# Optimization experiments

Measured on AMD Instinct MI355X. Metric: run time of the kernel, lower is better.

## Reference

```python
import jax, jax.numpy as jnp
import numpy as np

TEMPERATURE = 1.0
IGNORE_INDEX = -100


def setup_inputs() -> dict:
    key = jax.random.key(0)
    k1, k2, k3 = jax.random.split(key, 3)
    N, V = 8192, 32000
    Q, D = 8192, 512
    return {
        "input": jax.random.normal(k1, (N, V), dtype=jnp.float32),
        "label": jax.random.randint(k2, (N,), 0, V, dtype=jnp.int64),
        "query": jax.random.normal(k3, (Q, D), dtype=jnp.float32),
    }


def _cross_entropy(logits, label):
    # nn.CrossEntropyLoss(ignore_index=IGNORE_INDEX): mean NLL over non-ignored.
    logp = jax.nn.log_softmax(logits, axis=-1)
    safe_label = jnp.clip(label, 0, logits.shape[-1] - 1)
    nll = -jnp.take_along_axis(logp, safe_label[:, None], axis=-1)[:, 0]
    valid = (label != IGNORE_INDEX)
    num_valid = jnp.maximum(jnp.sum(valid), 1)
    return jnp.sum(jnp.where(valid, nll, 0.0)) / num_valid.astype(logits.dtype)


def _query_similarity_penalty(query, temperature):
    sq_norm = jnp.sum(query * query, axis=-1)  # [Q]
    sq = sq_norm[:, None] + sq_norm[None, :] - 2.0 * (query @ query.T)
    sq = jnp.maximum(sq, 0.0)
    dist = jnp.sqrt(jnp.where(sq > 0.0, sq, 1.0))
    dist = jnp.where(sq > 0.0, dist, 0.0)  # exact 0 on diagonal
    sim = jnp.exp(-dist / temperature)
    return jnp.sqrt(jnp.sum(sim * sim))  # Frobenius norm


def reference(input, label, query):
    ce = _cross_entropy(input, label)
    penalty = _query_similarity_penalty(query, TEMPERATURE)
    return ce + penalty
```

## Files before the change

kernel.cpp:

```cpp
#include <hip/hip_runtime.h>
#include <hip/hip_bf16.h>
#include <cstdint>

typedef unsigned short u16;
typedef __attribute__((ext_vector_type(8))) short short8;
typedef __attribute__((ext_vector_type(4))) float floatx4;

#define IGNORE_INDEX (-100)

__global__ __launch_bounds__(64) void init_acc(float* acc) {
    if (threadIdx.x < 3) acc[threadIdx.x] = 0.f;
}

__global__ __launch_bounds__(256) void prep_kernel(const float* __restrict__ q,
                                                   u16* __restrict__ qb,
                                                   float* __restrict__ nrm) {
    const int gwave = (blockIdx.x * 256 + threadIdx.x) >> 6;
    const int lane  = threadIdx.x & 63;
    const float4* src = (const float4*)(q + (size_t)gwave * 512);
    float4 a = src[lane * 2];
    float4 b = src[lane * 2 + 1];
    float v[8] = {a.x, a.y, a.z, a.w, b.x, b.y, b.z, b.w};
    float ss = 0.f;
    union { u16 u[8]; uint4 p; } pk;
#pragma unroll
    for (int t = 0; t < 8; ++t) {
        ss += v[t] * v[t];
        __hip_bfloat16 h = __float2bfloat16(v[t]);
        pk.u[t] = *(u16*)&h;
    }
    ((uint4*)qb)[(size_t)gwave * 64 + lane] = pk.p;
#pragma unroll
    for (int off = 32; off; off >>= 1) ss += __shfl_down(ss, off);
    if (lane == 0) nrm[gwave] = ss;
}

#define GLD16(g, l) __builtin_amdgcn_global_load_lds(                          \
    (const __attribute__((address_space(1))) void*)(g),                        \
    (__attribute__((address_space(3))) void*)(l), 16, 0, 0)

__global__ __launch_bounds__(256, 2) void fused_kernel(const u16* __restrict__ qb,
                                                       const float* __restrict__ nrm,
                                                       const float* __restrict__ x,
                                                       const int* __restrict__ lab,
                                                       float* __restrict__ accs,
                                                       int V, int tiles_per_side) {
    __shared__ __align__(16) u16 At[128 * 64];
    __shared__ __align__(16) u16 Bt[128 * 64];
    __shared__ float red[4];
    const int bid  = blockIdx.x;
    const int tid  = threadIdx.x;
    const int lane = tid & 63;
    const int w    = tid >> 6;

    if (bid % 3 == 0) {
        const int t  = bid / 3;
        const int i0 = (t / tiles_per_side) * 128;
        const int j0 = (t % tiles_per_side) * 128;
        const int wr = w >> 1, wc = w & 1;
        const int m15 = lane & 15, quad = lane >> 4;

        floatx4 acc[4][4];
#pragma unroll
        for (int a = 0; a < 4; ++a)
#pragma unroll
            for (int b = 0; b < 4; ++b) acc[a][b] = (floatx4)0.f;

        for (int kt = 0; kt < 8; ++kt) {
            const int k0 = kt * 64;
#pragma unroll
            for (int it = 0; it < 4; ++it) {
                int c   = it * 256 + tid;
                int row = c >> 3;
                int kc  = (c & 7) ^ (row & 7);
                const u16* ga = qb + (size_t)(i0 + row) * 512 + k0 + kc * 8;
                const u16* gb = qb + (size_t)(j0 + row) * 512 + k0 + kc * 8;
                GLD16(ga, &At[c * 8]);
                GLD16(gb, &Bt[c * 8]);
            }
            __syncthreads();
#pragma unroll
            for (int ks = 0; ks < 2; ++ks) {
                const int kcq = ks * 4 + quad;
                short8 af[4], bfr[4];
#pragma unroll
                for (int f = 0; f < 4; ++f) {
                    int ra = wr * 64 + f * 16 + m15;
                    af[f]  = *(const short8*)&At[(ra * 8 + (kcq ^ (ra & 7))) * 8];
                    int rb = wc * 64 + f * 16 + m15;
                    bfr[f] = *(const short8*)&Bt[(rb * 8 + (kcq ^ (rb & 7))) * 8];
                }
#pragma unroll
                for (int fi = 0; fi < 4; ++fi)
#pragma unroll
                    for (int fj = 0; fj < 4; ++fj)
                        acc[fi][fj] = __builtin_amdgcn_mfma_f32_16x16x32_bf16(
                            af[fi], bfr[fj], acc[fi][fj], 0, 0, 0);
            }
            __syncthreads();
        }

        float ni[4][4], nj[4];
#pragma unroll
        for (int fi = 0; fi < 4; ++fi)
#pragma unroll
            for (int r = 0; r < 4; ++r)
                ni[fi][r] = nrm[i0 + wr * 64 + fi * 16 + quad * 4 + r];
#pragma unroll
        for (int fj = 0; fj < 4; ++fj) nj[fj] = nrm[j0 + wc * 64 + fj * 16 + m15];

        float lsum = 0.f;
#pragma unroll
        for (int fi = 0; fi < 4; ++fi) {
#pragma unroll
            for (int fj = 0; fj < 4; ++fj) {
#pragma unroll
                for (int r = 0; r < 4; ++r) {
                    int i = i0 + wr * 64 + fi * 16 + quad * 4 + r;
                    int j = j0 + wc * 64 + fj * 16 + m15;
                    float sq = ni[fi][r] + nj[fj] - 2.f * acc[fi][fj][r];
                    float s;
                    if (i == j) s = 1.f;
                    else if (sq > 0.f) s = __expf(-sqrtf(sq));
                    else s = 1.f;
                    lsum += s * s;
                }
            }
        }
#pragma unroll
        for (int off = 32; off; off >>= 1) lsum += __shfl_down(lsum, off);
        if (lane == 0) red[w] = lsum;
        __syncthreads();
        if (tid == 0) atomicAdd(&accs[0], red[0] + red[1] + red[2] + red[3]);
    } else {
        const int row = bid - bid / 3 - 1;
        const float* xr = x + (size_t)row * V;
        float s = 0.f;
        const int nvec = V >> 2;
        const float4* xv = (const float4*)xr;
        for (int idx = tid; idx < nvec; idx += 256) {
            float4 v = xv[idx];
            s += __expf(v.x) + __expf(v.y) + __expf(v.z) + __expf(v.w);
        }
        for (int idx = (nvec << 2) + tid; idx < V; idx += 256)
            s += __expf(xr[idx]);
#pragma unroll
        for (int off = 32; off; off >>= 1) s += __shfl_down(s, off);
        if (lane == 0) red[w] = s;
        __syncthreads();
        if (tid == 0) {
            float S = red[0] + red[1] + red[2] + red[3];
            int l = lab[row];
            if (l != IGNORE_INDEX) {
                float xl = xr[l];
                atomicAdd(&accs[1], __logf(S) - xl);
                atomicAdd(&accs[2], 1.f);
            }
        }
    }
}

__global__ void finalize_kernel(const float* __restrict__ accs, float* __restrict__ out) {
    out[0] = accs[1] / fmaxf(accs[2], 1.f) + sqrtf(accs[0]);
}

extern "C" void kernel_launch(void* const* d_in, const int* in_sizes, int n_in,
                              void* d_out, int out_size, void* d_ws, size_t ws_size,
                              hipStream_t stream) {
    const float* input = (const float*)d_in[0];
    const int*   label = (const int*)d_in[1];
    const float* query = (const float*)d_in[2];
    float* out = (float*)d_out;

    const int N = in_sizes[1];
    const int V = in_sizes[0] / N;
    const int D = 512;
    const int Q = in_sizes[2] / D;
    const int T = Q / 128;

    float* accs = (float*)d_ws;
    float* nrm  = (float*)((char*)d_ws + 4096);
    u16*   qb   = (u16*)  ((char*)d_ws + 4096 + 64 * 1024);

    hipLaunchKernelGGL(init_acc, dim3(1), dim3(64), 0, stream, accs);
    hipLaunchKernelGGL(prep_kernel, dim3(Q / 4), dim3(256), 0, stream, query, qb, nrm);
    hipLaunchKernelGGL(fused_kernel, dim3(T * T + N), dim3(256), 0, stream,
                       qb, nrm, input, label, accs, V, T);
    hipLaunchKernelGGL(finalize_kernel, dim3(1), dim3(1), 0, stream, accs, out);
}
```

Baseline: 1.417 ms.

## Exploit symmetry of distance matrix and unroll CE row reduction with nontemporal loads

The pairwise similarity sum now visits only upper-triangular tiles, doubling off-diagonal tile contributions, which roughly halves the GEMM and exp work. The interleave ratio between GEMM tiles and CE rows changes from 1:2 to 1:4 to keep the mix balanced, and excess CE blocks exit early. The CE row loop is unrolled 8-way with nontemporal vector loads and split accumulators, and the label gather is issued before the streaming loop. The linear search for the triangular tile index adds a small per-block cost.

```diff
diff --git a/kernel.cpp b/kernel.cpp
--- a/kernel.cpp
+++ b/kernel.cpp
@@ -44,7 +44,7 @@
                                                        const float* __restrict__ x,
                                                        const int* __restrict__ lab,
                                                        float* __restrict__ accs,
-                                                       int V, int tiles_per_side) {
+                                                       int V, int N, int tiles_per_side) {
     __shared__ __align__(16) u16 At[128 * 64];
     __shared__ __align__(16) u16 Bt[128 * 64];
     __shared__ float red[4];
@@ -53,10 +53,13 @@
     const int lane = tid & 63;
     const int w    = tid >> 6;
 
-    if (bid % 3 == 0) {
-        const int t  = bid / 3;
-        const int i0 = (t / tiles_per_side) * 128;
-        const int j0 = (t % tiles_per_side) * 128;
+    if (bid % 5 == 0) {
+        int t = bid / 5;
+        int ti = 0, rem = t;
+        while (rem >= tiles_per_side - ti) { rem -= tiles_per_side - ti; ++ti; }
+        const int tj = ti + rem;
+        const int i0 = ti * 128;
+        const int j0 = tj * 128;
         const int wr = w >> 1, wc = w & 1;
         const int m15 = lane & 15, quad = lane >> 4;
 
@@ -131,28 +134,53 @@
         for (int off = 32; off; off >>= 1) lsum += __shfl_down(lsum, off);
         if (lane == 0) red[w] = lsum;
         __syncthreads();
-        if (tid == 0) atomicAdd(&accs[0], red[0] + red[1] + red[2] + red[3]);
+        if (tid == 0) {
+            const float wgt = (ti == tj) ? 1.f : 2.f;
+            atomicAdd(&accs[0], wgt * (red[0] + red[1] + red[2] + red[3]));
+        }
     } else {
-        const int row = bid - bid / 3 - 1;
+        const int row = bid - bid / 5 - 1;
+        if (row >= N) return;
         const float* xr = x + (size_t)row * V;
-        float s = 0.f;
+
+        int l = 0; float xl = 0.f;
+        if (tid == 0) {
+            l = lab[row];
+            if (l != IGNORE_INDEX) xl = xr[l];
+        }
+
         const int nvec = V >> 2;
-        const float4* xv = (const float4*)xr;
-        for (int idx = tid; idx < nvec; idx += 256) {
-            float4 v = xv[idx];
-            s += __expf(v.x) + __expf(v.y) + __expf(v.z) + __expf(v.w);
-        }
-        for (int idx = (nvec << 2) + tid; idx < V; idx += 256)
-            s += __expf(xr[idx]);
+        const floatx4* __restrict__ xv = (const floatx4*)xr;
+        float s0 = 0.f, s1 = 0.f, s2 = 0.f, s3 = 0.f;
+        int idx = tid;
+        const int lim = nvec - 256 * 7;
+        for (; idx < lim; idx += 256 * 8) {
+            floatx4 v[8];
+#pragma unroll
+            for (int u = 0; u < 8; ++u)
+                v[u] = __builtin_nontemporal_load(xv + idx + 256 * u);
+#pragma unroll
+            for (int u = 0; u < 8; ++u) {
+                s0 += __expf(v[u].x);
+                s1 += __expf(v[u].y);
+                s2 += __expf(v[u].z);
+                s3 += __expf(v[u].w);
+            }
+        }
+        for (; idx < nvec; idx += 256) {
+            floatx4 v = __builtin_nontemporal_load(xv + idx);
+            s0 += __expf(v.x); s1 += __expf(v.y); s2 += __expf(v.z); s3 += __expf(v.w);
+        }
+        for (int t2 = (nvec << 2) + tid; t2 < V; t2 += 256)
+            s0 += __expf(xr[t2]);
+        float s = (s0 + s1) + (s2 + s3);
 #pragma unroll
         for (int off = 32; off; off >>= 1) s += __shfl_down(s, off);
         if (lane == 0) red[w] = s;
         __syncthreads();
         if (tid == 0) {
             float S = red[0] + red[1] + red[2] + red[3];
-            int l = lab[row];
             if (l != IGNORE_INDEX) {
-                float xl = xr[l];
                 atomicAdd(&accs[1], __logf(S) - xl);
                 atomicAdd(&accs[2], 1.f);
             }
@@ -177,6 +205,7 @@
     const int D = 512;
     const int Q = in_sizes[2] / D;
     const int T = Q / 128;
+    const int U = T * (T + 1) / 2;
 
     float* accs = (float*)d_ws;
     float* nrm  = (float*)((char*)d_ws + 4096);
@@ -184,7 +213,7 @@
 
     hipLaunchKernelGGL(init_acc, dim3(1), dim3(64), 0, stream, accs);
     hipLaunchKernelGGL(prep_kernel, dim3(Q / 4), dim3(256), 0, stream, query, qb, nrm);
-    hipLaunchKernelGGL(fused_kernel, dim3(T * T + N), dim3(256), 0, stream,
-                       qb, nrm, input, label, accs, V, T);
+    hipLaunchKernelGGL(fused_kernel, dim3(U * 5), dim3(256), 0, stream,
+                       qb, nrm, input, label, accs, V, N, T);
     hipLaunchKernelGGL(finalize_kernel, dim3(1), dim3(1), 0, stream, accs, out);
 }
```

After: 1.413 ms. No clear change (-0.3%).
